# Optimization experiments

Measured on AMD Instinct MI355X. Metric: run time of the kernel, lower is better.

## Reference

```python
import jax, jax.numpy as jnp
import numpy as np

N_NODES = 50000
N_EDGES = 800000
N_GRAPHS = 64
NEG_SLOPE = 0.2  # PyG GATConv default leaky_relu slope
EPS = 1e-16      # PyG softmax denominator epsilon


def gat_conv(x, W, a_src, a_dst, bias, src, dst, n_nodes):
    """PyG GATConv (heads=1, concat=True, self-loops already appended).
    x: [N, F_in], W: [F_in, H*F], a_src/a_dst: [H, F], bias: [H*F]."""
    H, F = a_src.shape
    h = (x @ W).reshape(-1, H, F)                      # [N, H, F]
    alpha_src = jnp.einsum('nhf,hf->nh', h, a_src)     # [N, H]
    alpha_dst = jnp.einsum('nhf,hf->nh', h, a_dst)     # [N, H]
    e = jax.nn.leaky_relu(alpha_src[src] + alpha_dst[dst], NEG_SLOPE)  # [E, H]
    # segment softmax over incoming edges of each destination node
    e_max = jax.ops.segment_max(e, dst, num_segments=n_nodes)          # [N, H]
    e_exp = jnp.exp(e - e_max[dst])
    denom = jax.ops.segment_sum(e_exp, dst, num_segments=n_nodes)      # [N, H]
    alpha = e_exp / (denom[dst] + EPS)                                 # [E, H]
    msg = alpha[:, :, None] * h[src]                                   # [E, H, F]
    out = jax.ops.segment_sum(msg, dst, num_segments=n_nodes)          # [N, H, F]
    return out.reshape(-1, H * F) + bias


def global_mean_pool(x, batch, n_graphs):
    s = jax.ops.segment_sum(x, batch, num_segments=n_graphs)
    cnt = jax.ops.segment_sum(jnp.ones((x.shape[0],), x.dtype), batch, num_segments=n_graphs)
    return s / jnp.maximum(cnt, 1.0)[:, None]


def setup_inputs() -> dict:
    key = jax.random.key(0)
    ks = jax.random.split(key, 10)
    d_in, d_h, d_out, L, H = 128, 128, 10, 3, 1
    x = jax.random.normal(ks[0], (N_NODES, d_in), dtype=jnp.float32)
    edge_index = jax.random.randint(ks[1], (2, N_EDGES), 0, N_NODES, dtype=jnp.int32)
    edge_attr = jax.random.normal(ks[2], (N_EDGES, 4), dtype=jnp.float32)
    batch = jnp.sort(jax.random.randint(ks[3], (N_NODES,), 0, N_GRAPHS, dtype=jnp.int32))
    s0 = 1.0 / np.sqrt(d_in)
    sh = 1.0 / np.sqrt(d_h)
    return {
        'x': x,
        'edge_index': edge_index,
        'edge_attr': edge_attr,
        'batch': batch,
        'W0': jax.random.normal(ks[4], (d_in, d_h), dtype=jnp.float32) * s0,
        'b0': jnp.zeros((d_h,), jnp.float32),
        'Wc': jax.random.normal(ks[5], (L, d_h, H * d_h), dtype=jnp.float32) * sh,
        'att_src': jax.random.normal(ks[6], (L, H, d_h), dtype=jnp.float32) * sh,
        'att_dst': jax.random.normal(ks[7], (L, H, d_h), dtype=jnp.float32) * sh,
        'bc': jnp.zeros((L, H * d_h), jnp.float32),
        'W1': jax.random.normal(ks[8], (d_h, d_out), dtype=jnp.float32) * sh,
        'b1': jnp.zeros((d_out,), jnp.float32),
    }


def reference(x, edge_index, edge_attr, batch, W0, b0, Wc, att_src, att_dst, bc, W1, b1):
    n = x.shape[0]
    # GATConv default add_self_loops=True
    loops = jnp.arange(n, dtype=edge_index.dtype)
    src = jnp.concatenate([edge_index[0], loops])
    dst = jnp.concatenate([edge_index[1], loops])
    # dropout p=0 / eval mode -> identity
    h = jax.nn.relu(x @ W0 + b0)
    for i in range(Wc.shape[0]):
        h = jax.nn.relu(gat_conv(h, Wc[i], att_src[i], att_dst[i], bc[i], src, dst, n))
    pooled = global_mean_pool(h, batch, N_GRAPHS)   # [B, d_h]
    return pooled @ W1 + b1                          # [B, d_out]
```

## Files before the change

kernel.cpp:

```cpp
#include <hip/hip_runtime.h>
#include <hip/hip_bf16.h>
#include <hip/hip_fp16.h>
#include <hip/hip_fp8.h>

#define NN 50000
#define NE 800000
#define NG 64
#define DH 128

#define NPB 256
#define NBK ((NN + NPB - 1) / NPB)
#define EPB 4096
#define NPBLK ((NE + EPB - 1) / EPB)
#define CAPB 5120
#define GEMMB 782
#define CST 136
#define CSTB 136
#define SMEM_BYTES 18432

#if defined(__has_builtin)
# if __has_builtin(__builtin_amdgcn_cvt_pk_f32_fp8) && __has_builtin(__builtin_amdgcn_cvt_pk_fp8_f32)
#  define HW_FP8 1
# endif
#endif

typedef __bf16 bfx8 __attribute__((ext_vector_type(8)));
typedef float  f32x4 __attribute__((ext_vector_type(4)));

__device__ __forceinline__ ushort f2b(float f) {
    unsigned b = __float_as_uint(f);
    b += 0x7fff + ((b >> 16) & 1);
    return (ushort)(b >> 16);
}
__device__ __forceinline__ float b2f(ushort s) {
    return __uint_as_float((unsigned)s << 16);
}
__device__ __forceinline__ unsigned pk2(float a, float b) {
    return (unsigned)f2b(a) | ((unsigned)f2b(b) << 16);
}

__device__ __forceinline__ unsigned f2fp8(float v) {
    v = fminf(fmaxf(v, -448.f), 448.f);
#ifdef HW_FP8
    return (unsigned)__builtin_amdgcn_cvt_pk_fp8_f32(v, v, 0, false) & 0xFFu;
#else
    __hip_fp8_e4m3 t(v);
    return (unsigned)*(const unsigned char*)&t;
#endif
}
__device__ __forceinline__ void fp8x4_up(unsigned u, float* o) {
#ifdef HW_FP8
    auto lo = __builtin_amdgcn_cvt_pk_f32_fp8((int)u, false);
    auto hi = __builtin_amdgcn_cvt_pk_f32_fp8((int)u, true);
    o[0] = lo[0]; o[1] = lo[1]; o[2] = hi[0]; o[3] = hi[1];
#else
    #pragma unroll
    for (int k = 0; k < 4; ++k) {
        unsigned char c = (u >> (8 * k)) & 0xFF;
        o[k] = float(*(const __hip_fp8_e4m3*)&c);
    }
#endif
}

__launch_bounds__(256)
__global__ void k_partwt(const int* __restrict__ ei, int* __restrict__ gcur,
                         unsigned* __restrict__ tmp,
                         const float* __restrict__ W0, const float* __restrict__ Wc,
                         ushort* __restrict__ Wt) {
    int t = threadIdx.x;
    if (blockIdx.x >= NPBLK) {
        int i = (blockIdx.x - NPBLK) * 256 + t;
        int m = i >> 14;
        int r = i & 16383;
        int k = r >> 7, n = r & 127;
        const float* src = (m == 0) ? W0 : (Wc + (size_t)(m - 1) * DH * DH);
        Wt[(size_t)m * DH * DH + n * DH + k] = f2b(src[r]);
        return;
    }
    __shared__ int cnt[NBK], base[NBK], lcur[NBK];
    for (int i = t; i < NBK; i += 256) cnt[i] = 0;
    __syncthreads();
    int e0 = blockIdx.x * EPB;
    int dreg[16];
    #pragma unroll
    for (int j = 0; j < 16; ++j) {
        int e = e0 + j * 256 + t;
        dreg[j] = (e < NE) ? ei[NE + e] : -1;
        if (e < NE) atomicAdd(&cnt[dreg[j] >> 8], 1);
    }
    __syncthreads();
    for (int i = t; i < NBK; i += 256) {
        base[i] = cnt[i] ? atomicAdd(&gcur[i], cnt[i]) : 0;
        lcur[i] = 0;
    }
    __syncthreads();
    #pragma unroll
    for (int j = 0; j < 16; ++j) {
        int e = e0 + j * 256 + t;
        if (e < NE) {
            int d = dreg[j], s = ei[e];
            int b = d >> 8;
            int r = atomicAdd(&lcur[b], 1);
            tmp[(size_t)b * CAPB + base[b] + r] = ((unsigned)(d & 255) << 16) | (unsigned)s;
        }
    }
}

__launch_bounds__(256)
__global__ void k_bcount(const unsigned* __restrict__ tmp, const int* __restrict__ gcur,
                         int* __restrict__ deg, int* __restrict__ ploc,
                         int* __restrict__ bsizeP) {
    __shared__ int dcnt[NPB];
    int b = blockIdx.x, t = threadIdx.x;
    dcnt[t] = 0;
    __syncthreads();
    int ne = gcur[b];
    for (int e = t; e < ne; e += 256)
        atomicAdd(&dcnt[tmp[(size_t)b * CAPB + e] >> 16], 1);
    __syncthreads();
    int n = b * NPB + t;
    int d = (n < NN) ? dcnt[t] : 0;
    int p = (n < NN) ? ((d + 4) & ~3) : 0;
    int inc = p;
    #pragma unroll
    for (int off = 1; off < 64; off <<= 1) {
        int u = __shfl_up(inc, off);
        if ((t & 63) >= off) inc += u;
    }
    __shared__ int wsum[4];
    if ((t & 63) == 63) wsum[t >> 6] = inc;
    __syncthreads();
    int w = t >> 6, woff = 0;
    #pragma unroll
    for (int k = 0; k < 4; ++k) if (k < w) woff += wsum[k];
    int lofs = inc - p + woff;
    if (n < NN) { deg[n] = d; ploc[n] = lofs; }
    if (t == 255) bsizeP[b] = lofs + p;
}

template<bool AF32, bool DOTS, bool OUTFP8>
__device__ __forceinline__ void gemm_body(char* smem, int gblk,
        const void* __restrict__ Av, const ushort* __restrict__ Wt,
        const float* __restrict__ bias, void* __restrict__ C, int relu,
        const float* __restrict__ avs, const float* __restrict__ avd,
        float* __restrict__ asrc, float* __restrict__ adst) {
    int tid = threadIdx.x;
    int wid = (gblk * 256 + tid) >> 6;
    int lane = tid & 63;
    int row0 = wid * 16;
    if (row0 >= NN) return;
    int mrow = lane & 15;
    int quad = lane >> 4;
    int arow = row0 + mrow;

    f32x4 acc[8];
    #pragma unroll
    for (int t = 0; t < 8; ++t)
        #pragma unroll
        for (int r = 0; r < 4; ++r) acc[t][r] = 0.f;

    #pragma unroll
    for (int ks = 0; ks < 4; ++ks) {
        int k0 = ks * 32 + quad * 8;
        bfx8 a;
        if (AF32) {
            const float* ap = (const float*)Av + (size_t)arow * DH + k0;
            union { ushort s[8]; bfx8 v; } u;
            #pragma unroll
            for (int j = 0; j < 8; ++j) u.s[j] = f2b(ap[j]);
            a = u.v;
        } else {
            a = *(const bfx8*)((const ushort*)Av + (size_t)arow * DH + k0);
        }
        #pragma unroll
        for (int t = 0; t < 8; ++t) {
            bfx8 b = *(const bfx8*)(Wt + (size_t)(t * 16 + mrow) * DH + k0);
            acc[t] = __builtin_amdgcn_mfma_f32_16x16x32_bf16(a, b, acc[t], 0, 0, 0);
        }
    }

    if (OUTFP8) {
        uchar* my = (uchar*)smem + (tid >> 6) * 16 * CSTB;
        #pragma unroll
        for (int t = 0; t < 8; ++t) {
            int col = t * 16 + mrow;
            float bv = bias ? bias[col] : 0.f;
            #pragma unroll
            for (int r = 0; r < 4; ++r) {
                float v = acc[t][r] + bv;
                if (relu) v = fmaxf(v, 0.f);
                my[(quad * 4 + r) * CSTB + col] = (uchar)f2fp8(v);
            }
        }
        #pragma unroll
        for (int i = 0; i < 4; ++i) {
            int idx = i * 64 + lane;
            int row = idx >> 4;
            int c8 = idx & 15;
            uint2 u = *(const uint2*)(my + row * CSTB + c8 * 8);
            *(uint2*)((uchar*)C + (size_t)(row0 + row) * DH + c8 * 8) = u;
        }
    } else {
        ushort* my = (ushort*)smem + (tid >> 6) * 16 * CST;
        #pragma unroll
        for (int t = 0; t < 8; ++t) {
            int col = t * 16 + mrow;
            float bv = bias ? bias[col] : 0.f;
            #pragma unroll
            for (int r = 0; r < 4; ++r) {
                float v = acc[t][r] + bv;
                if (relu) v = fmaxf(v, 0.f);
                my[(quad * 4 + r) * CST + col] = f2b(v);
            }
        }
        #pragma unroll
        for (int i = 0; i < 4; ++i) {
            int idx = i * 64 + lane;
            int row = idx >> 4;
            int c16 = idx & 15;
            uint4 u = *(const uint4*)(my + row * CST + c16 * 8);
            *(uint4*)((ushort*)C + (size_t)(row0 + row) * DH + c16 * 8) = u;
        }
    }

    if (DOTS) {
        float av[8], dv[8];
        #pragma unroll
        for (int t = 0; t < 8; ++t) {
            av[t] = avs[t * 16 + mrow];
            dv[t] = avd[t * 16 + mrow];
        }
        int orow = row0 + quad * 4;
        #pragma unroll
        for (int r = 0; r < 4; ++r) {
            float ps = 0.f, pd = 0.f;
            #pragma unroll
            for (int t = 0; t < 8; ++t) {
                ps += acc[t][r] * av[t];
                pd += acc[t][r] * dv[t];
            }
            #pragma unroll
            for (int off = 1; off < 16; off <<= 1) {
                ps += __shfl_xor(ps, off);
                pd += __shfl_xor(pd, off);
            }
            if (mrow == 0) {
                asrc[orow + r] = ps;
                adst[orow + r] = pd;
            }
        }
    }
}

__launch_bounds__(256)
__global__ void k_buildgemm(const unsigned* __restrict__ tmp, const int* __restrict__ gcur,
                            const int* __restrict__ bsizeP, const int* __restrict__ ploc,
                            int* __restrict__ pstart, ushort* __restrict__ csr,
                            const float* __restrict__ x, const ushort* __restrict__ Wt,
                            const float* __restrict__ b0, ushort* __restrict__ hB) {
    __shared__ char smem[SMEM_BYTES];
    int t = threadIdx.x;
    if (blockIdx.x < GEMMB) {
        gemm_body<true, false, false>(smem, blockIdx.x, x, Wt, b0, hB, 1,
                                      nullptr, nullptr, nullptr, nullptr);
        return;
    }
    int b = blockIdx.x - GEMMB;
    ushort* buf = (ushort*)smem;
    int* lcur = (int*)(smem + 16384);
    int* sm   = (int*)(smem + 16384 + 1024);
    int v = (t < NBK) ? bsizeP[t] : 0;
    sm[t] = v;
    __syncthreads();
    for (int off = 1; off < 256; off <<= 1) {
        int u = (t >= off) ? sm[t - off] : 0;
        __syncthreads();
        sm[t] += u;
        __syncthreads();
    }
    int r0 = sm[b] - bsizeP[b];
    int S = bsizeP[b];
    int n0 = b * NPB, n1 = min(n0 + NPB, NN), nodes = n1 - n0;
    int ne = gcur[b];

    if (S <= 8192) {
        for (int i = t; i < (S >> 1); i += 256) ((unsigned*)buf)[i] = 0;
        __syncthreads();
        if (t < nodes) {
            int lp = ploc[n0 + t];
            pstart[n0 + t] = r0 + lp;
            lcur[t] = lp + 1;
            buf[lp] = (ushort)(n0 + t);
        }
        __syncthreads();
        for (int e = t; e < ne; e += 256) {
            unsigned u = tmp[(size_t)b * CAPB + e];
            int slot = atomicAdd(&lcur[u >> 16], 1);
            buf[slot] = (ushort)(u & 0xffffu);
        }
        __syncthreads();
        unsigned* dst = (unsigned*)(csr + r0);
        for (int i = t; i < (S >> 1); i += 256) dst[i] = ((unsigned*)buf)[i];
    } else {
        for (int i = t; i < S; i += 256) csr[r0 + i] = 0;
        __syncthreads();
        if (t < nodes) {
            int lp = ploc[n0 + t];
            pstart[n0 + t] = r0 + lp;
            lcur[t] = r0 + lp + 1;
            csr[r0 + lp] = (ushort)(n0 + t);
        }
        __syncthreads();
        for (int e = t; e < ne; e += 256) {
            unsigned u = tmp[(size_t)b * CAPB + e];
            int slot = atomicAdd(&lcur[u >> 16], 1);
            csr[slot] = (ushort)(u & 0xffffu);
        }
    }
}

__launch_bounds__(256)
__global__ void k_gemmdots(const ushort* __restrict__ hB, const ushort* __restrict__ Wt,
                           uchar* __restrict__ hA,
                           const float* __restrict__ avs, const float* __restrict__ avd,
                           float* __restrict__ asrc, float* __restrict__ adst) {
    __shared__ char smem[SMEM_BYTES];
    gemm_body<false, true, true>(smem, blockIdx.x, hB, Wt, nullptr, hA, 0,
                                 avs, avd, asrc, adst);
}

__launch_bounds__(256)
__global__ void k_aggr(const uchar* __restrict__ h8, const float* __restrict__ asrc,
                       const float* __restrict__ adst, const int* __restrict__ pstart,
                       const int* __restrict__ deg, const ushort* __restrict__ csr,
                       const float* __restrict__ bias, ushort* __restrict__ hout) {
    int wid = (blockIdx.x * blockDim.x + threadIdx.x) >> 6;
    int lane = threadIdx.x & 63;
    if (wid >= NN) return;
    int start = pstart[wid];
    int cnt = deg[wid] + 1;
    float ad = adst[wid];

    if (cnt <= 64) {
        int s = csr[start + lane];
        float e = -1e30f;
        if (lane < cnt) {
            float t = asrc[s] + ad;
            e = fmaxf(t, 0.f) + 0.2f * fminf(t, 0.f);
        }
        float m = e;
        #pragma unroll
        for (int off = 32; off; off >>= 1) m = fmaxf(m, __shfl_xor(m, off));
        float w = (lane < cnt) ? __expf(e - m) : 0.f;
        float dsum = w;
        #pragma unroll
        for (int off = 32; off; off >>= 1) dsum += __shfl_xor(dsum, off);

        int g = lane >> 4, fidx = lane & 15;
        float acc[8];
        #pragma unroll
        for (int k = 0; k < 8; ++k) acc[k] = 0.f;

        int steps = (cnt + 3) >> 2;
        const uint2* hp = (const uint2*)h8;
        int j = 0;
        for (; j + 3 < steps; j += 4) {
            int   e0 = j * 4 + g,      e1 = e0 + 4,  e2 = e0 + 8,  e3 = e0 + 12;
            float w0 = __shfl(w, e0),  w1 = __shfl(w, e1);
            float w2 = __shfl(w, e2),  w3 = __shfl(w, e3);
            int   s0 = __shfl(s, e0),  s1 = __shfl(s, e1);
            int   s2 = __shfl(s, e2),  s3 = __shfl(s, e3);
            uint2 u0 = hp[(size_t)s0 * 16 + fidx];
            uint2 u1 = hp[(size_t)s1 * 16 + fidx];
            uint2 u2 = hp[(size_t)s2 * 16 + fidx];
            uint2 u3 = hp[(size_t)s3 * 16 + fidx];
            float v[8];
            fp8x4_up(u0.x, v); fp8x4_up(u0.y, v + 4);
            #pragma unroll
            for (int k = 0; k < 8; ++k) acc[k] += w0 * v[k];
            fp8x4_up(u1.x, v); fp8x4_up(u1.y, v + 4);
            #pragma unroll
            for (int k = 0; k < 8; ++k) acc[k] += w1 * v[k];
            fp8x4_up(u2.x, v); fp8x4_up(u2.y, v + 4);
            #pragma unroll
            for (int k = 0; k < 8; ++k) acc[k] += w2 * v[k];
            fp8x4_up(u3.x, v); fp8x4_up(u3.y, v + 4);
            #pragma unroll
            for (int k = 0; k < 8; ++k) acc[k] += w3 * v[k];
        }
        for (; j < steps; ++j) {
            int e0 = j * 4 + g;
            float w0 = __shfl(w, e0);
            int   s0 = __shfl(s, e0);
            uint2 u0 = hp[(size_t)s0 * 16 + fidx];
            float v[8];
            fp8x4_up(u0.x, v); fp8x4_up(u0.y, v + 4);
            #pragma unroll
            for (int k = 0; k < 8; ++k) acc[k] += w0 * v[k];
        }
        #pragma unroll
        for (int k = 0; k < 8; ++k) {
            acc[k] += __shfl_xor(acc[k], 16);
            acc[k] += __shfl_xor(acc[k], 32);
        }
        if (g == 0) {
            float inv = 1.f / (dsum + 1e-16f);
            const float4* bp = (const float4*)bias;
            float4 b0 = bp[fidx * 2], b1 = bp[fidx * 2 + 1];
            uint4 o;
            o.x = pk2(fmaxf(acc[0] * inv + b0.x, 0.f), fmaxf(acc[1] * inv + b0.y, 0.f));
            o.y = pk2(fmaxf(acc[2] * inv + b0.z, 0.f), fmaxf(acc[3] * inv + b0.w, 0.f));
            o.z = pk2(fmaxf(acc[4] * inv + b1.x, 0.f), fmaxf(acc[5] * inv + b1.y, 0.f));
            o.w = pk2(fmaxf(acc[6] * inv + b1.z, 0.f), fmaxf(acc[7] * inv + b1.w, 0.f));
            ((uint4*)hout)[(size_t)wid * 16 + fidx] = o;
        }
        return;
    }

    float m = -1e30f;
    for (int i0 = start; i0 < start + cnt; i0 += 64) {
        int i = i0 + lane;
        float e = -1e30f;
        if (i < start + cnt) {
            int s = csr[i];
            float t = asrc[s] + ad;
            e = fmaxf(t, 0.f) + 0.2f * fminf(t, 0.f);
        }
        m = fmaxf(m, e);
    }
    #pragma unroll
    for (int off = 32; off; off >>= 1) m = fmaxf(m, __shfl_xor(m, off));

    float accx = 0.f, accy = 0.f, dsum = 0.f;
    for (int i0 = start; i0 < start + cnt; i0 += 64) {
        int i = i0 + lane;
        int s = 0; float w = 0.f;
        if (i < start + cnt) {
            s = csr[i];
            float t = asrc[s] + ad;
            float e = fmaxf(t, 0.f) + 0.2f * fminf(t, 0.f);
            w = __expf(e - m);
        }
        dsum += w;
        int cl = min(64, start + cnt - i0);
        for (int j = 0; j < cl; ++j) {
            int   sj = __shfl(s, j);
            float wj = __shfl(w, j);
            unsigned us = *(const ushort*)(h8 + (size_t)sj * DH + lane * 2);
            float v[4];
            fp8x4_up(us, v);
            accx += wj * v[0];
            accy += wj * v[1];
        }
    }
    #pragma unroll
    for (int off = 32; off; off >>= 1) dsum += __shfl_xor(dsum, off);

    float inv = 1.f / (dsum + 1e-16f);
    float ox = fmaxf(accx * inv + bias[lane * 2], 0.f);
    float oy = fmaxf(accy * inv + bias[lane * 2 + 1], 0.f);
    *(unsigned*)(hout + (size_t)wid * DH + lane * 2) = pk2(ox, oy);
}

__launch_bounds__(256)
__global__ void k_pool(const ushort* __restrict__ h, const int* __restrict__ batch,
                       float* __restrict__ gsum, int* __restrict__ gcnt) {
    int slot = threadIdx.x >> 7;
    int f = threadIdx.x & 127;
    int n0 = blockIdx.x * 64;
    int n1 = min(n0 + 64, NN);
    int first = n0 + slot;
    if (first >= n1) return;
    int g0 = batch[n0], g1 = batch[n1 - 1];
    if (g0 == g1) {
        float acc = 0.f;
        for (int nd = first; nd < n1; nd += 2)
            acc += b2f(h[(size_t)nd * DH + f]);
        atomicAdd(&gsum[g0 * DH + f], acc);
        if (f == 0 && slot == 0) atomicAdd(&gcnt[g0], n1 - n0);
        return;
    }
    float acc = 0.f; int run = 0;
    int gcur = batch[first];
    for (int nd = first; nd < n1; nd += 2) {
        int g = batch[nd];
        if (g != gcur) {
            atomicAdd(&gsum[gcur * DH + f], acc);
            if (f == 0) atomicAdd(&gcnt[gcur], run);
            acc = 0.f; run = 0; gcur = g;
        }
        acc += b2f(h[(size_t)nd * DH + f]);
        run += 1;
    }
    atomicAdd(&gsum[gcur * DH + f], acc);
    if (f == 0) atomicAdd(&gcnt[gcur], run);
}

__global__ void k_final(const float* __restrict__ gsum, const int* __restrict__ gcnt,
                        const float* __restrict__ W1, const float* __restrict__ b1,
                        float* __restrict__ out) {
    int t = threadIdx.x;
    if (t >= NG * 10) return;
    int g = t / 10, o = t % 10;
    float inv = 1.f / fmaxf((float)gcnt[g], 1.f);
    float acc = 0.f;
    for (int f = 0; f < DH; ++f) acc += gsum[g * DH + f] * W1[f * 10 + o];
    out[t] = acc * inv + b1[o];
}

extern "C" void kernel_launch(void* const* d_in, const int* in_sizes, int n_in,
                              void* d_out, int out_size, void* d_ws, size_t ws_size,
                              hipStream_t stream) {
    const float* x       = (const float*)d_in[0];
    const int*   ei      = (const int*)d_in[1];
    const int*   batch   = (const int*)d_in[3];
    const float* W0      = (const float*)d_in[4];
    const float* b0      = (const float*)d_in[5];
    const float* Wc      = (const float*)d_in[6];
    const float* att_src = (const float*)d_in[7];
    const float* att_dst = (const float*)d_in[8];
    const float* bc      = (const float*)d_in[9];
    const float* W1      = (const float*)d_in[10];
    const float* b1      = (const float*)d_in[11];
    float* out = (float*)d_out;

    char* ws = (char*)d_ws;
    size_t off = 0;
    auto alloc = [&](size_t bytes) {
        void* p = ws + off;
        off += (bytes + 255) & ~(size_t)255;
        return p;
    };
    uchar*    hA     = (uchar*)alloc((size_t)NN * DH);
    ushort*   hB     = (ushort*)alloc((size_t)NN * DH * 2);
    ushort*   Wt     = (ushort*)alloc((size_t)4 * DH * DH * 2);
    int*      pstart = (int*)alloc((size_t)NN * 4);
    ushort*   csr    = (ushort*)alloc((size_t)(NE + 4 * NN + 64) * 2);
    unsigned* tmp    = (unsigned*)alloc((size_t)NBK * CAPB * 4);
    float*    asrc   = (float*)alloc(NN * 4);
    float*    adst   = (float*)alloc(NN * 4);
    int*      deg    = (int*)alloc(NN * 4);
    int*      ploc   = (int*)alloc(NN * 4);
    int*      gcur   = (int*)alloc((NBK + 1) * 4);
    int*      bsizeP = (int*)alloc((NBK + 1) * 4);
    float*    gsum   = (float*)alloc(NG * DH * 4);
    int*      gcnt   = (int*)alloc(NG * 4);

    hipMemsetAsync(gcur, 0, (NBK + 1) * 4, stream);
    hipMemsetAsync(gsum, 0, NG * DH * 4 + 256, stream);

    k_partwt<<<NPBLK + 256, 256, 0, stream>>>(ei, gcur, tmp, W0, Wc, Wt);
    k_bcount<<<NBK, 256, 0, stream>>>(tmp, gcur, deg, ploc, bsizeP);
    k_buildgemm<<<GEMMB + NBK, 256, 0, stream>>>(tmp, gcur, bsizeP, ploc, pstart, csr,
                                                 x, Wt, b0, hB);

    for (int l = 0; l < 3; ++l) {
        k_gemmdots<<<GEMMB, 256, 0, stream>>>(hB, Wt + (size_t)(l + 1) * DH * DH, hA,
                                              att_src + l * DH, att_dst + l * DH,
                                              asrc, adst);
        k_aggr<<<(NN + 3) / 4, 256, 0, stream>>>(hA, asrc, adst, pstart, deg, csr,
                                                 bc + l * DH, hB);
    }

    k_pool<<<(NN + 63) / 64, 256, 0, stream>>>(hB, batch, gsum, gcnt);
    k_final<<<1, NG * 10, 0, stream>>>(gsum, gcnt, W1, b1, out);
}
```

Baseline: 323.2 us.

## Make GEMM waves persistent with register-resident weight fragments

The dense GEMM body now uses a fixed grid of 512 blocks. Each wave loads all 32 weight fragments into registers once, then grid-strides over 16-row tiles instead of handling a single tile. A-row loads for all four K-steps are issued up front as wide vector loads before the MFMAs. This amortizes weight reloads and adds memory-level parallelism, at the cost of many more VGPRs (about 128 for B fragments alone), which may lower occupancy. The change also alters the block count that the fused build kernel uses to split GEMM blocks from the other blocks.

```diff
diff --git a/kernel.cpp b/kernel.cpp
--- a/kernel.cpp
+++ b/kernel.cpp
@@ -13,7 +13,8 @@
 #define EPB 4096
 #define NPBLK ((NE + EPB - 1) / EPB)
 #define CAPB 5120
-#define GEMMB 782
+#define GEMMB 512
+#define GEMMW (GEMMB * 4)
 #define CST 136
 #define CSTB 136
 #define SMEM_BYTES 18432
@@ -26,6 +27,7 @@
 
 typedef __bf16 bfx8 __attribute__((ext_vector_type(8)));
 typedef float  f32x4 __attribute__((ext_vector_type(4)));
+typedef float  f32x8 __attribute__((ext_vector_type(8)));
 
 __device__ __forceinline__ ushort f2b(float f) {
     unsigned b = __float_as_uint(f);
@@ -144,109 +146,128 @@
         const float* __restrict__ bias, void* __restrict__ C, int relu,
         const float* __restrict__ avs, const float* __restrict__ avd,
         float* __restrict__ asrc, float* __restrict__ adst) {
+    const int NT = NN / 16;
     int tid = threadIdx.x;
-    int wid = (gblk * 256 + tid) >> 6;
     int lane = tid & 63;
-    int row0 = wid * 16;
-    if (row0 >= NN) return;
     int mrow = lane & 15;
     int quad = lane >> 4;
-    int arow = row0 + mrow;
-
-    f32x4 acc[8];
-    #pragma unroll
-    for (int t = 0; t < 8; ++t)
-        #pragma unroll
-        for (int r = 0; r < 4; ++r) acc[t][r] = 0.f;
-
+    int wid = (gblk * 256 + tid) >> 6;
+
+    bfx8 b[4][8];
     #pragma unroll
     for (int ks = 0; ks < 4; ++ks) {
         int k0 = ks * 32 + quad * 8;
-        bfx8 a;
-        if (AF32) {
-            const float* ap = (const float*)Av + (size_t)arow * DH + k0;
-            union { ushort s[8]; bfx8 v; } u;
-            #pragma unroll
-            for (int j = 0; j < 8; ++j) u.s[j] = f2b(ap[j]);
-            a = u.v;
-        } else {
-            a = *(const bfx8*)((const ushort*)Av + (size_t)arow * DH + k0);
-        }
-        #pragma unroll
-        for (int t = 0; t < 8; ++t) {
-            bfx8 b = *(const bfx8*)(Wt + (size_t)(t * 16 + mrow) * DH + k0);
-            acc[t] = __builtin_amdgcn_mfma_f32_16x16x32_bf16(a, b, acc[t], 0, 0, 0);
-        }
-    }
-
-    if (OUTFP8) {
-        uchar* my = (uchar*)smem + (tid >> 6) * 16 * CSTB;
-        #pragma unroll
-        for (int t = 0; t < 8; ++t) {
-            int col = t * 16 + mrow;
-            float bv = bias ? bias[col] : 0.f;
-            #pragma unroll
-            for (int r = 0; r < 4; ++r) {
-                float v = acc[t][r] + bv;
-                if (relu) v = fmaxf(v, 0.f);
-                my[(quad * 4 + r) * CSTB + col] = (uchar)f2fp8(v);
-            }
-        }
-        #pragma unroll
-        for (int i = 0; i < 4; ++i) {
-            int idx = i * 64 + lane;
-            int row = idx >> 4;
-            int c8 = idx & 15;
-            uint2 u = *(const uint2*)(my + row * CSTB + c8 * 8);
-            *(uint2*)((uchar*)C + (size_t)(row0 + row) * DH + c8 * 8) = u;
-        }
-    } else {
-        ushort* my = (ushort*)smem + (tid >> 6) * 16 * CST;
-        #pragma unroll
-        for (int t = 0; t < 8; ++t) {
-            int col = t * 16 + mrow;
-            float bv = bias ? bias[col] : 0.f;
-            #pragma unroll
-            for (int r = 0; r < 4; ++r) {
-                float v = acc[t][r] + bv;
-                if (relu) v = fmaxf(v, 0.f);
-                my[(quad * 4 + r) * CST + col] = f2b(v);
-            }
-        }
-        #pragma unroll
-        for (int i = 0; i < 4; ++i) {
-            int idx = i * 64 + lane;
-            int row = idx >> 4;
-            int c16 = idx & 15;
-            uint4 u = *(const uint4*)(my + row * CST + c16 * 8);
-            *(uint4*)((ushort*)C + (size_t)(row0 + row) * DH + c16 * 8) = u;
-        }
-    }
-
+        #pragma unroll
+        for (int t = 0; t < 8; ++t)
+            b[ks][t] = *(const bfx8*)(Wt + (size_t)(t * 16 + mrow) * DH + k0);
+    }
+    float av[8], dv[8];
     if (DOTS) {
-        float av[8], dv[8];
         #pragma unroll
         for (int t = 0; t < 8; ++t) {
             av[t] = avs[t * 16 + mrow];
             dv[t] = avd[t * 16 + mrow];
         }
-        int orow = row0 + quad * 4;
-        #pragma unroll
-        for (int r = 0; r < 4; ++r) {
-            float ps = 0.f, pd = 0.f;
+    }
+
+    for (int tile = wid; tile < NT; tile += GEMMW) {
+        int row0 = tile * 16;
+        int arow = row0 + mrow;
+
+        bfx8 a[4];
+        if (AF32) {
+            f32x8 af[4];
+            #pragma unroll
+            for (int ks = 0; ks < 4; ++ks)
+                af[ks] = *(const f32x8*)((const float*)Av + (size_t)arow * DH + ks * 32 + quad * 8);
+            #pragma unroll
+            for (int ks = 0; ks < 4; ++ks) {
+                union { ushort s[8]; bfx8 v; } u;
+                #pragma unroll
+                for (int j = 0; j < 8; ++j) u.s[j] = f2b(af[ks][j]);
+                a[ks] = u.v;
+            }
+        } else {
+            #pragma unroll
+            for (int ks = 0; ks < 4; ++ks)
+                a[ks] = *(const bfx8*)((const ushort*)Av + (size_t)arow * DH + ks * 32 + quad * 8);
+        }
+
+        f32x4 acc[8];
+        #pragma unroll
+        for (int t = 0; t < 8; ++t)
+            #pragma unroll
+            for (int r = 0; r < 4; ++r) acc[t][r] = 0.f;
+
+        #pragma unroll
+        for (int ks = 0; ks < 4; ++ks)
+            #pragma unroll
+            for (int t = 0; t < 8; ++t)
+                acc[t] = __builtin_amdgcn_mfma_f32_16x16x32_bf16(a[ks], b[ks][t], acc[t], 0, 0, 0);
+
+        if (OUTFP8) {
+            uchar* my = (uchar*)smem + (tid >> 6) * 16 * CSTB;
             #pragma unroll
             for (int t = 0; t < 8; ++t) {
-                ps += acc[t][r] * av[t];
-                pd += acc[t][r] * dv[t];
+                int col = t * 16 + mrow;
+                float bv = bias ? bias[col] : 0.f;
+                #pragma unroll
+                for (int r = 0; r < 4; ++r) {
+                    float v = acc[t][r] + bv;
+                    if (relu) v = fmaxf(v, 0.f);
+                    my[(quad * 4 + r) * CSTB + col] = (uchar)f2fp8(v);
+                }
             }
             #pragma unroll
-            for (int off = 1; off < 16; off <<= 1) {
-                ps += __shfl_xor(ps, off);
-                pd += __shfl_xor(pd, off);
+            for (int i = 0; i < 4; ++i) {
+                int idx = i * 64 + lane;
+                int row = idx >> 4;
+                int c8 = idx & 15;
+                uint2 u = *(const uint2*)(my + row * CSTB + c8 * 8);
+                *(uint2*)((uchar*)C + (size_t)(row0 + row) * DH + c8 * 8) = u;
             }
-            if (mrow == 0) {
-                asrc[orow + r] = ps;
-                adst[orow + r] = pd;
+        } else {
+            ushort* my = (ushort*)smem + (tid >> 6) * 16 * CST;
+            #pragma unroll
+            for (int t = 0; t < 8; ++t) {
+                int col = t * 16 + mrow;
+                float bv = bias ? bias[col] : 0.f;
+                #pragma unroll
+                for (int r = 0; r < 4; ++r) {
+                    float v = acc[t][r] + bv;
+                    if (relu) v = fmaxf(v, 0.f);
+                    my[(quad * 4 + r) * CST + col] = f2b(v);
+                }
+            }
+            #pragma unroll
+            for (int i = 0; i < 4; ++i) {
+                int idx = i * 64 + lane;
+                int row = idx >> 4;
+                int c16 = idx & 15;
+                uint4 u = *(const uint4*)(my + row * CST + c16 * 8);
+                *(uint4*)((ushort*)C + (size_t)(row0 + row) * DH + c16 * 8) = u;
+            }
+        }
+
+        if (DOTS) {
+            int orow = row0 + quad * 4;
+            #pragma unroll
+            for (int r = 0; r < 4; ++r) {
+                float ps = 0.f, pd = 0.f;
+                #pragma unroll
+                for (int t = 0; t < 8; ++t) {
+                    ps += acc[t][r] * av[t];
+                    pd += acc[t][r] * dv[t];
+                }
+                #pragma unroll
+                for (int off = 1; off < 16; off <<= 1) {
+                    ps += __shfl_xor(ps, off);
+                    pd += __shfl_xor(pd, off);
+                }
+                if (mrow == 0) {
+                    asrc[orow + r] = ps;
+                    adst[orow + r] = pd;
+                }
             }
         }
     }
```

Measured after the change: 309.2 us. 4.3% less time.
